# Performance work log

Hardware: AMD Instinct MI355X
Metric: run time of the kernel (lower is better)

The kernel has to match this reference:

```python
import jax, jax.numpy as jnp
import numpy as np

B, T, D = 8, 512, 1024
S, H, TOPK = 2048, 4, 8
Dh = D // H
LR_FAST, LR_DEEP = 1.0, 0.1
SURPRISE_TH, DECAY = 0.6, 0.9995


def layer_norm(x, g, b, eps=1e-5):
    m = jnp.mean(x, -1, keepdims=True)
    v = jnp.var(x, -1, keepdims=True)
    return (x - m) * jax.lax.rsqrt(v + eps) * g + b


def setup_inputs() -> dict:
    key = jax.random.key(0)
    ks = jax.random.split(key, 8)
    s = 0.02
    f32 = jnp.float32
    return {
        "x": jax.random.normal(ks[0], (B, T, D), f32),
        "write_mask": jnp.ones((B, T), dtype=bool),
        # Mamba backbone stub: 2 residual MLP blocks (Linear d->2d, GELU, Linear 2d->d, LN)
        "W1": jax.random.normal(ks[1], (2, D, 2 * D), f32) * s,
        "b1": jnp.zeros((2, 2 * D), f32),
        "W2": jax.random.normal(ks[2], (2, 2 * D, D), f32) * s,
        "b2": jnp.zeros((2, D), f32),
        "ln_g": jnp.ones((2, D), f32),
        "ln_b": jnp.zeros((2, D), f32),
        # memory fusion
        "fuse_W": jax.random.normal(ks[3], (2 * D, D), f32) * s,
        "fuse_b": jnp.zeros((D,), f32),
        "mln_g": jnp.ones((D,), f32),
        "mln_b": jnp.zeros((D,), f32),
        # persistent DualTierMiras memory bank (keys / values)
        "mem_K": jax.random.normal(ks[4], (S, D), f32) * s,
        "mem_V": jax.random.normal(ks[5], (S, D), f32) * s,
    }


def _forward(x, write_mask, W1, b1, W2, b2, ln_g, ln_b, fuse_W, fuse_b, mln_g, mln_b, mem_K, mem_V):
    # --- Mamba backbone (vectorized over B,T) ---
    h = x
    for i in range(2):
        y = jax.nn.gelu(h @ W1[i] + b1[i]) @ W2[i] + b2[i]
        h = h + layer_norm(y, ln_g[i], ln_b[i])

    inv_sqrt_dh = 1.0 / np.sqrt(Dh).astype(np.float32)
    inv_sqrt_d = 1.0 / np.sqrt(D).astype(np.float32)

    def step(carry, inputs):
        mK, mV = carry                      # [S,D] each
        h_t, m_t = inputs                   # [B,D], [B] bool
        # --- top-k sparse multi-head memory read ---
        q = h_t.reshape(B, H, Dh)
        Kh = mK.reshape(S, H, Dh).transpose(1, 0, 2)   # [H,S,Dh]
        Vh = mV.reshape(S, H, Dh).transpose(1, 0, 2)   # [H,S,Dh]
        scores = jnp.einsum('bhd,hsd->bhs', q, Kh) * inv_sqrt_dh  # [B,H,S]
        topv, topi = jax.lax.top_k(scores, TOPK)                   # [B,H,K]
        w = jax.nn.softmax(topv, axis=-1)
        vals = jax.vmap(lambda v, i: v[i])(Vh, topi.transpose(1, 0, 2))  # [H,B,K,Dh]
        v_t = jnp.einsum('bhk,hbkd->bhd', w, vals).reshape(B, D)
        # --- residual fusion ---
        fused = jnp.concatenate([h_t, v_t], -1) @ fuse_W + fuse_b
        fused = layer_norm(fused + h_t, mln_g, mln_b)
        # --- surprise-gated EMA scatter write (detached, decayed) ---
        key_w = jax.lax.stop_gradient(h_t)
        val_w = jax.lax.stop_gradient(fused)
        sw = key_w @ mK.T * inv_sqrt_d                 # [B,S]
        p = jax.nn.softmax(sw, -1)
        slot = jnp.argmax(sw, -1)                      # [B]
        surprise = 1.0 - jnp.max(p, -1)                # [B]
        lr = jnp.where(surprise > SURPRISE_TH, LR_FAST, LR_DEEP)
        lr = lr * m_t.astype(lr.dtype)                 # per-sample write gate
        decay = jnp.where(jnp.any(m_t), DECAY, 1.0)
        mV2 = mV * decay
        mV2 = mV2.at[slot].add(lr[:, None] * (val_w - mV2[slot]))
        mK2 = mK.at[slot].add(lr[:, None] * (key_w - mK[slot]))
        return (mK2, mV2), fused

    (_, _), out = jax.lax.scan(step, (mem_K, mem_V), (h.transpose(1, 0, 2), write_mask.T))
    return out.transpose(1, 0, 2)   # [B,T,D]


def reference(x, write_mask, W1, b1, W2, b2, ln_g, ln_b, fuse_W, fuse_b, mln_g, mln_b, mem_K, mem_V):
    return _forward(x, write_mask, W1, b1, W2, b2, ln_g, ln_b, fuse_W, fuse_b, mln_g, mln_b, mem_K, mem_V)
```

## Files before the change

kernel.cpp:

```cpp
#include <hip/hip_runtime.h>
#include <cstdint>

#define TT 512
#define DD 1024
#define SS 2048
#define BB 8
#define DECAYF 0.9995f
#define NBLK 256

__device__ __forceinline__ float cldf(const float* p) {
  return __hip_atomic_load(p, __ATOMIC_RELAXED, __HIP_MEMORY_SCOPE_AGENT);
}
__device__ __forceinline__ void cstf(float* p, float v) {
  __hip_atomic_store(p, v, __ATOMIC_RELAXED, __HIP_MEMORY_SCOPE_AGENT);
}
__device__ __forceinline__ int cldi(const int* p) {
  return __hip_atomic_load(p, __ATOMIC_RELAXED, __HIP_MEMORY_SCOPE_AGENT);
}
__device__ __forceinline__ void csti(int* p, int v) {
  __hip_atomic_store(p, v, __ATOMIC_RELAXED, __HIP_MEMORY_SCOPE_AGENT);
}

template<int MODE, bool BT>
__global__ __launch_bounds__(256) void gemm64(
    const float* __restrict__ A, int lda,
    const float* __restrict__ B, int ldb,
    const float* __restrict__ bias,
    float* __restrict__ C, int ldc,
    const float* __restrict__ res, int resld,
    int K)
{
  __shared__ float As[16][68];
  __shared__ float Bs[16][68];
  const int tid = threadIdx.x;
  const int m0 = blockIdx.y * 64, n0 = blockIdx.x * 64;
  const int tx = tid & 15, ty = tid >> 4;
  const int a_r = tid >> 2, a_k = (tid & 3) * 4;
  const int b_k = tid >> 4, b_n = (tid & 15) * 4;
  float acc[4][4];
#pragma unroll
  for (int i = 0; i < 4; ++i)
#pragma unroll
    for (int j = 0; j < 4; ++j) acc[i][j] = 0.f;

  for (int k0 = 0; k0 < K; k0 += 16) {
    float4 av = *(const float4*)(A + (size_t)(m0 + a_r) * lda + k0 + a_k);
    As[a_k + 0][a_r] = av.x; As[a_k + 1][a_r] = av.y;
    As[a_k + 2][a_r] = av.z; As[a_k + 3][a_r] = av.w;
    if (!BT) {
      float4 bv = *(const float4*)(B + (size_t)(k0 + b_k) * ldb + n0 + b_n);
      Bs[b_k][b_n + 0] = bv.x; Bs[b_k][b_n + 1] = bv.y;
      Bs[b_k][b_n + 2] = bv.z; Bs[b_k][b_n + 3] = bv.w;
    } else {
      float4 bv = *(const float4*)(B + (size_t)(n0 + a_r) * ldb + k0 + a_k);
      Bs[a_k + 0][a_r] = bv.x; Bs[a_k + 1][a_r] = bv.y;
      Bs[a_k + 2][a_r] = bv.z; Bs[a_k + 3][a_r] = bv.w;
    }
    __syncthreads();
#pragma unroll
    for (int kk = 0; kk < 16; ++kk) {
      float4 a4 = *(const float4*)&As[kk][ty * 4];
      float4 b4 = *(const float4*)&Bs[kk][tx * 4];
      float aa[4] = {a4.x, a4.y, a4.z, a4.w};
      float bb[4] = {b4.x, b4.y, b4.z, b4.w};
#pragma unroll
      for (int i = 0; i < 4; ++i)
#pragma unroll
        for (int j = 0; j < 4; ++j) acc[i][j] += aa[i] * bb[j];
    }
    __syncthreads();
  }
#pragma unroll
  for (int i = 0; i < 4; ++i) {
    const int row = m0 + ty * 4 + i;
    const int col = n0 + tx * 4;
    float v[4];
#pragma unroll
    for (int j = 0; j < 4; ++j) {
      float x = acc[i][j];
      if (MODE == 0 || MODE == 1 || MODE == 3) x += bias[col + j];
      if (MODE == 1) {
        float t3 = x * x * x;
        x = 0.5f * x * (1.f + tanhf(0.7978845608028654f * (x + 0.044715f * t3)));
      }
      if (MODE == 3) x += res[(size_t)row * resld + col + j];
      v[j] = x;
    }
    float4 o; o.x = v[0]; o.y = v[1]; o.z = v[2]; o.w = v[3];
    *(float4*)(C + (size_t)row * ldc + col) = o;
  }
}

__global__ __launch_bounds__(256) void ln_residual(
    const float* __restrict__ Y, float* __restrict__ Hio,
    const float* __restrict__ g, const float* __restrict__ b)
{
  const int row = blockIdx.x, tid = threadIdx.x;
  const int lane = tid & 63, wid = tid >> 6;
  __shared__ float red[8];
  __shared__ float s_m, s_r;
  float x[4]; float ls = 0.f, lq = 0.f;
#pragma unroll
  for (int r = 0; r < 4; ++r) {
    x[r] = Y[(size_t)row * DD + tid + 256 * r];
    ls += x[r]; lq += x[r] * x[r];
  }
#pragma unroll
  for (int off = 32; off; off >>= 1) { ls += __shfl_down(ls, off); lq += __shfl_down(lq, off); }
  if (lane == 0) { red[wid] = ls; red[4 + wid] = lq; }
  __syncthreads();
  if (tid == 0) {
    float S = red[0] + red[1] + red[2] + red[3];
    float Q = red[4] + red[5] + red[6] + red[7];
    float mean = S * (1.f / 1024.f);
    float var = Q * (1.f / 1024.f) - mean * mean;
    s_m = mean; s_r = rsqrtf(var + 1e-5f);
  }
  __syncthreads();
#pragma unroll
  for (int r = 0; r < 4; ++r) {
    int d = tid + 256 * r;
    Hio[(size_t)row * DD + d] += (x[r] - s_m) * s_r * g[d] + b[d];
  }
}

__device__ __forceinline__ void waitn(const int* a, int n, int tgt) {
  if (threadIdx.x < n) {
    while (cldi(&a[threadIdx.x * 32]) < tgt) __builtin_amdgcn_s_sleep(4);
  }
  __syncthreads();
}
__device__ __forceinline__ void arrive1(int* a, int idx, int val) {
  __syncthreads();
  if (threadIdx.x == 0) csti(&a[idx * 32], val);
}

__device__ __forceinline__ void load_qv(float4 (&qv)[8][4], const float* H,
                                        int trow, int lane) {
#pragma unroll
  for (int b = 0; b < 8; ++b)
#pragma unroll
    for (int k = 0; k < 4; ++k)
      qv[b][k] = *(const float4*)(H + ((size_t)b * TT + trow) * DD + lane * 16 + k * 4);
}

__device__ __forceinline__ void compute_scores(
    const float4 (&qv)[8][4], const float* Kl, int bid,
    float* SgP, float* pmxP, float* s_ph, float* s_fd)
{
  const int tid = threadIdx.x, lane = tid & 63, wid = tid >> 6;
  const float4* K4 = (const float4*)Kl;
#pragma unroll
  for (int si = 0; si < 2; ++si) {
    const int sloc = wid * 2 + si;
    float4 kf[4];
#pragma unroll
    for (int k = 0; k < 4; ++k) kf[k] = K4[sloc * 256 + (k << 6) + lane];
    float acc[8];
#pragma unroll
    for (int b = 0; b < 8; ++b) {
      float a = 0.f;
#pragma unroll
      for (int k = 0; k < 4; ++k) {
        a += qv[b][k].x * kf[k].x; a += qv[b][k].y * kf[k].y;
        a += qv[b][k].z * kf[k].z; a += qv[b][k].w * kf[k].w;
      }
      acc[b] = a;
    }
#pragma unroll
    for (int lvl = 1; lvl <= 8; lvl <<= 1)
#pragma unroll
      for (int b = 0; b < 8; ++b) acc[b] += __shfl_xor(acc[b], lvl);
#pragma unroll
    for (int b = 0; b < 8; ++b)
      if ((lane & 15) == b) s_ph[sloc * 32 + (b << 2) + (lane >> 4)] = acc[b];
#pragma unroll
    for (int b = 0; b < 8; ++b) {
      float s1 = acc[b] + __shfl_xor(acc[b], 16);
      s1 += __shfl_xor(s1, 32);
      if (lane == b) s_fd[sloc * 8 + b] = s1;
    }
  }
  __syncthreads();
  {
    const int row = tid >> 3, col = tid & 7;
    cstf(&SgP[(size_t)row * SS + bid * 8 + col], s_ph[col * 32 + row]);
  }
  if (tid < 8) {
    float m = -3e38f; int ix = 0;
#pragma unroll
    for (int s = 0; s < 8; ++s) { float v = s_fd[s * 8 + tid]; if (v > m) { m = v; ix = bid * 8 + s; } }
    float e = 0.f;
#pragma unroll
    for (int s = 0; s < 8; ++s) e += __expf((s_fd[s * 8 + tid] - m) * 0.03125f);
    float* rec = &pmxP[bid * 32];
    cstf(&rec[tid], m); cstf(&rec[8 + tid], e); csti((int*)&rec[16 + tid], ix);
  }
}

__device__ __forceinline__ void fuse_ln_out(
    int b, int tl,
    const float* __restrict__ HP, const float* part,
    float* __restrict__ H, float* pvalP,
    const float* __restrict__ mg, const float* __restrict__ mb,
    float* xr, float* s_red)
{
  const int tid = threadIdx.x;
  const int lane = tid & 63, wid = tid >> 6;
  const size_t row = (size_t)b * TT + tl;
  float ls = 0.f, lq = 0.f;
#pragma unroll
  for (int r = 0; r < 4; ++r) {
    int d = tid + 256 * r;
    float x = HP[row * DD + d]
            + cldf(&part[(0 * 8 + b) * DD + d]) + cldf(&part[(1 * 8 + b) * DD + d])
            + cldf(&part[(2 * 8 + b) * DD + d]) + cldf(&part[(3 * 8 + b) * DD + d]);
    xr[d] = x; ls += x; lq += x * x;
  }
#pragma unroll
  for (int off = 32; off; off >>= 1) { ls += __shfl_down(ls, off); lq += __shfl_down(lq, off); }
  if (lane == 0) { s_red[wid] = ls; s_red[4 + wid] = lq; }
  __syncthreads();
  if (tid == 0) {
    float S = s_red[0] + s_red[1] + s_red[2] + s_red[3];
    float Q = s_red[4] + s_red[5] + s_red[6] + s_red[7];
    float mean = S * (1.f / 1024.f);
    float var = Q * (1.f / 1024.f) - mean * mean;
    s_red[8] = mean; s_red[9] = rsqrtf(var + 1e-5f);
  }
  __syncthreads();
  const float mean = s_red[8], rstd = s_red[9];
#pragma unroll
  for (int r = 0; r < 4; ++r) {
    int d = tid + 256 * r;
    float val = (xr[d] - mean) * rstd * mg[d] + mb[d];
    H[row * DD + d] = val;
    cstf(&pvalP[b * DD + d], val);
  }
}

__global__ __launch_bounds__(256) void scan_kernel(
    float* __restrict__ H, const float* __restrict__ HP, float* U,
    float* Sg3, float* pmx2, float* vt2, float* coefg2, float* part, float* pval2,
    int* arrA, int* arrT, int* arrC, int* arrD, int* arrE,
    const float* __restrict__ memK, const float* __restrict__ fuseW,
    const float* __restrict__ mg, const float* __restrict__ mb)
{
  __shared__ float Kl[8192];
  __shared__ float scr[4352];
  __shared__ float s_ph[256];
  __shared__ float s_fd[64];
  __shared__ float s_red[64];
  __shared__ int   s_redi[32];
  __shared__ float s_M[8];
  __shared__ int   s_MI[8];
  __shared__ float s_tkv[8];
  __shared__ int   s_tki[8];
  __shared__ int   s_ist[2][8];
  __shared__ float s_lr[2][8];

  const int bid = blockIdx.x, tid = threadIdx.x;
  const int lane = tid & 63, wid = tid >> 6;

  if (tid < 8) { s_ist[1][tid] = -1; s_lr[1][tid] = 0.f; }
  {
    float4* K4 = (float4*)Kl;
    const int s0 = bid * 8;
    for (int i = tid; i < 2048; i += 256) {
      int r = i >> 8, c = i & 255;
      K4[r * 256 + ((c & 3) << 6) + (c >> 2)] =
          *(const float4*)(memK + (size_t)(s0 + r) * DD + 4 * c);
    }
  }
  __syncthreads();

  float cr = 1.f;
  float4 qv[8][4];
  load_qv(qv, H, 0, lane);
  compute_scores(qv, Kl, bid, Sg3 , pmx2 , s_ph, s_fd);
  arrive1(arrA, bid, 1);

  for (int t = 0; t < TT; ++t) {
    const int p = t & 1, pp = p ^ 1;
    waitn(arrA, NBLK, t + 1);
    {
      const float* rec = &pmx2[p * 8192 + tid * 32];
      float pm8[8], pe8[8]; int ix8[8];
#pragma unroll
      for (int b = 0; b < 8; ++b) {
        pm8[b] = cldf(&rec[b]); pe8[b] = cldf(&rec[8 + b]);
        ix8[b] = cldi((const int*)&rec[16 + b]);
      }
#pragma unroll
      for (int b = 0; b < 8; ++b) {
        float M = pm8[b]; int MI = ix8[b];
#pragma unroll
        for (int off = 1; off < 64; off <<= 1) {
          float om = __shfl_xor(M, off); int oi = __shfl_xor(MI, off);
          if (om > M || (om == M && oi < MI)) { M = om; MI = oi; }
        }
        if (lane == 0) { s_red[wid * 8 + b] = M; s_redi[wid * 8 + b] = MI; }
      }
      __syncthreads();
      if (tid < 8) {
        float M = s_red[tid]; int MI = s_redi[tid];
#pragma unroll
        for (int w2 = 1; w2 < 4; ++w2) {
          float om = s_red[w2 * 8 + tid]; int oi = s_redi[w2 * 8 + tid];
          if (om > M || (om == M && oi < MI)) { M = om; MI = oi; }
        }
        s_M[tid] = M; s_MI[tid] = MI;
      }
      __syncthreads();
#pragma unroll
      for (int b = 0; b < 8; ++b) {
        float term = pe8[b] * __expf((pm8[b] - s_M[b]) * 0.03125f);
#pragma unroll
        for (int off = 1; off < 64; off <<= 1) term += __shfl_xor(term, off);
        if (lane == 0) s_red[wid * 8 + b] = term;
      }
      __syncthreads();
      if (tid < 8) {
        float seg = s_red[tid] + s_red[8 + tid] + s_red[16 + tid] + s_red[24 + tid];
        float surprise = 1.f - 1.f / seg;
        s_lr[p][tid] = (surprise > 0.6f) ? 1.0f : 0.1f;
        s_ist[p][tid] = s_MI[tid];
      }
      __syncthreads();
    }
    {
      int sl[8]; float lr8[8];
#pragma unroll
      for (int e = 0; e < 8; ++e) { sl[e] = s_ist[p][e]; lr8[e] = s_lr[p][e]; }
      const int s0 = bid * 8;
      float4* K4 = (float4*)Kl;
#pragma unroll
      for (int si = 0; si < 2; ++si) {
        const int sloc = wid * 2 + si, s = s0 + sloc;
        float L = 0.f; bool any = false;
        float4 av[4];
#pragma unroll
        for (int k = 0; k < 4; ++k) { av[k].x = 0.f; av[k].y = 0.f; av[k].z = 0.f; av[k].w = 0.f; }
#pragma unroll
        for (int e = 0; e < 8; ++e) {
          if (sl[e] == s) {
            any = true; L += lr8[e];
#pragma unroll
            for (int k = 0; k < 4; ++k) {
              av[k].x += lr8[e] * qv[e][k].x; av[k].y += lr8[e] * qv[e][k].y;
              av[k].z += lr8[e] * qv[e][k].z; av[k].w += lr8[e] * qv[e][k].w;
            }
          }
        }
        if (any) {
#pragma unroll
          for (int k = 0; k < 4; ++k) {
            float4 kv = K4[sloc * 256 + (k << 6) + lane];
            kv.x = kv.x * (1.f - L) + av[k].x;
            kv.y = kv.y * (1.f - L) + av[k].y;
            kv.z = kv.z * (1.f - L) + av[k].z;
            kv.w = kv.w * (1.f - L) + av[k].w;
            K4[sloc * 256 + (k << 6) + lane] = kv;
          }
        }
      }
    }
    __syncthreads();
    if (t < TT - 1) {
      load_qv(qv, H, t + 1, lane);
      compute_scores(qv, Kl, bid, Sg3 + (size_t)((t + 1) % 3) * 65536,
                     pmx2 + pp * 8192, s_ph, s_fd);
      arrive1(arrA, bid, t + 2);
    }
    if (bid < 32) {
      waitn(arrE, 8, t - 1);
      const float* SgR = &Sg3[(size_t)(t % 3) * 65536 + (size_t)bid * SS];
      float* sc = scr;
#pragma unroll
      for (int j = 0; j < 8; ++j) sc[tid + 256 * j] = cldf(&SgR[tid + 256 * j]);
      __syncthreads();
      if (wid == 0) {
        float a[32];
#pragma unroll
        for (int i = 0; i < 32; ++i) a[i] = sc[lane + 64 * i];
        unsigned msk = 0u;
        for (int r = 0; r < 8; ++r) {
          float bv = -3e38f; int bj = 0;
#pragma unroll
          for (int i = 0; i < 32; ++i) {
            bool ok = !((msk >> i) & 1u) && (a[i] > bv);
            bv = ok ? a[i] : bv;
            bj = ok ? i : bj;
          }
          int bidx = lane + 64 * bj;
#pragma unroll
          for (int off = 1; off < 64; off <<= 1) {
            float ov = __shfl_xor(bv, off);
            int oi = __shfl_xor(bidx, off);
            if (ov > bv || (ov == bv && oi < bidx)) { bv = ov; bidx = oi; }
          }
          if (lane == (bidx & 63)) msk |= 1u << (bidx >> 6);
          if (lane == 0) { s_tkv[r] = bv; s_tki[r] = bidx; }
        }
      }
      __syncthreads();
      float w8[8];
      {
        float mx = s_tkv[0], nrm = 0.f;
#pragma unroll
        for (int j = 0; j < 8; ++j) { w8[j] = __expf((s_tkv[j] - mx) * 0.0625f); nrm += w8[j]; }
        float scale = cr / nrm;
#pragma unroll
        for (int j = 0; j < 8; ++j) w8[j] *= scale;
      }
      int psl[8]; float plr[8];
#pragma unroll
      for (int e = 0; e < 8; ++e) { psl[e] = s_ist[pp][e]; plr[e] = s_lr[pp][e]; }
      const int b = bid >> 2, h = bid & 3;
      float accv = 0.f;
#pragma unroll
      for (int j = 0; j < 8; ++j) {
        int idx = s_tki[j];
        float uval = cldf(&U[(size_t)idx * DD + h * 256 + tid]);
        float L = 0.f;
#pragma unroll
        for (int e = 0; e < 8; ++e) L += (psl[e] == idx) ? plr[e] : 0.f;
        accv += w8[j] * uval * (1.f - L);
      }
      cstf(&vt2[p * 8192 + b * 1024 + h * 256 + tid], accv);
      if (tid < 8) {
        int myslot = psl[tid]; float mylr = plr[tid];
        float ce = 0.f;
#pragma unroll
        for (int j = 0; j < 8; ++j) ce += (s_tki[j] == myslot) ? w8[j] : 0.f;
        cstf(&coefg2[p * 256 + b * 32 + h * 8 + tid], ce * mylr * (1.f / cr));
      }
      arrive1(arrT, bid, t + 1);
    } else if (bid < 96) {
      waitn(arrT, 32, t + 1);
      waitn(arrD, 8, t);
      const int idx = bid - 32, g = idx >> 2, kc = idx & 3;
      float* vtl = scr; float* pr = scr + 2048; float* cfs = scr + 4096;
      cfs[tid] = cldf(&coefg2[p * 256 + tid]);
      float pv[8];
#pragma unroll
      for (int e = 0; e < 8; ++e) pv[e] = cldf(&pval2[pp * 8192 + e * DD + kc * 256 + tid]);
      __syncthreads();
#pragma unroll
      for (int r = 0; r < 8; ++r) {
        float v = cldf(&vt2[p * 8192 + r * DD + kc * 256 + tid]);
#pragma unroll
        for (int e = 0; e < 8; ++e) v += cfs[r * 32 + kc * 8 + e] * pv[e];
        vtl[r * 256 + tid] = v;
      }
      __syncthreads();
      const int colq = tid & 63, ksub = tid >> 6;
      const int col = 64 * g + colq;
      float acc[8];
#pragma unroll
      for (int b2 = 0; b2 < 8; ++b2) acc[b2] = 0.f;
      const float* W2 = fuseW + (size_t)(DD + kc * 256 + ksub * 64) * DD + col;
      const float* vl = vtl + ksub * 64;
      for (int kk = 0; kk < 64; ++kk) {
        float wv = W2[(size_t)kk * DD];
#pragma unroll
        for (int b2 = 0; b2 < 8; ++b2) acc[b2] += vl[b2 * 256 + kk] * wv;
      }
#pragma unroll
      for (int b2 = 0; b2 < 8; ++b2) pr[ksub * 512 + colq * 8 + b2] = acc[b2];
      __syncthreads();
      if (ksub == 0) {
#pragma unroll
        for (int b2 = 0; b2 < 8; ++b2) {
          float s2 = pr[colq * 8 + b2] + pr[512 + colq * 8 + b2]
                   + pr[1024 + colq * 8 + b2] + pr[1536 + colq * 8 + b2];
          cstf(&part[(kc * 8 + b2) * DD + col], s2);
        }
      }
      arrive1(arrC, idx, t + 1);
    } else if (bid < 104) {
      if (t >= 1) {
        waitn(arrC, 64, t);
        waitn(arrE, 8, t - 2);
        fuse_ln_out(bid - 96, t - 1, HP, part, H, pval2 + pp * 8192, mg, mb, scr, s_red);
        arrive1(arrD, bid - 96, t);
      }
    } else if (bid < 112) {
      if (t >= 1) {
        waitn(arrT, 32, t + 1);
        waitn(arrD, 8, t);
        int sl[8]; float lr8[8];
#pragma unroll
        for (int e2 = 0; e2 < 8; ++e2) { sl[e2] = s_ist[pp][e2]; lr8[e2] = s_lr[pp][e2]; }
        const int e = bid - 104, s = sl[e];
        bool owner = true;
        for (int e2 = 0; e2 < e; ++e2) if (sl[e2] == s) owner = false;
        if (owner) {
          float L = 0.f;
#pragma unroll
          for (int e2 = 0; e2 < 8; ++e2) if (sl[e2] == s) L += lr8[e2];
          const float psv = 1.f / cr;
#pragma unroll
          for (int r = 0; r < 4; ++r) {
            int d = tid + 256 * r;
            float add = 0.f;
#pragma unroll
            for (int e2 = 0; e2 < 8; ++e2)
              if (sl[e2] == s) add += lr8[e2] * cldf(&pval2[pp * 8192 + e2 * DD + d]);
            size_t o = (size_t)s * DD + d;
            cstf(&U[o], cldf(&U[o]) * (1.f - L) + psv * add);
          }
        }
        arrive1(arrE, bid - 104, t);
      }
    }
    cr *= DECAYF;
  }
  if (bid >= 96 && bid < 104) {
    waitn(arrC, 64, TT);
    waitn(arrE, 8, TT - 2);
    fuse_ln_out(bid - 96, TT - 1, HP, part, H, pval2 + ((TT - 1) & 1) * 8192,
                mg, mb, scr, s_red);
  }
}

extern "C" void kernel_launch(void* const* d_in, const int* in_sizes, int n_in,
                              void* d_out, int out_size, void* d_ws, size_t ws_size,
                              hipStream_t stream) {
  (void)in_sizes; (void)n_in; (void)out_size; (void)ws_size;
  const float* x     = (const float*)d_in[0];
  const float* W1    = (const float*)d_in[2];
  const float* b1    = (const float*)d_in[3];
  const float* W2    = (const float*)d_in[4];
  const float* b2    = (const float*)d_in[5];
  const float* lng   = (const float*)d_in[6];
  const float* lnb   = (const float*)d_in[7];
  const float* fuseW = (const float*)d_in[8];
  const float* fuseB = (const float*)d_in[9];
  const float* mlng  = (const float*)d_in[10];
  const float* mlnb  = (const float*)d_in[11];
  const float* memK  = (const float*)d_in[12];
  const float* memV  = (const float*)d_in[13];

  float* H = (float*)d_out;
  char* w = (char*)d_ws;
  float* Y1   = (float*)w;
  float* Y2   = (float*)(w + (size_t)32 * 1024 * 1024);
  float* HP   = (float*)(w + (size_t)48 * 1024 * 1024);
  float* U    = (float*)(w + (size_t)64 * 1024 * 1024);
  float* Sg3  = (float*)(w + (size_t)72 * 1024 * 1024);
  char*  db   = w + (size_t)73 * 1024 * 1024;
  float* pmx2   = (float*)db;
  float* vt2    = (float*)(db + 65536);
  float* coefg2 = (float*)(db + 131072);
  float* part   = (float*)(db + 196608);
  float* pval2  = (float*)(db + 327680);
  char*  fl   = w + (size_t)74 * 1024 * 1024;
  int* arrA = (int*)(fl);
  int* arrT = (int*)(fl + 32768);
  int* arrC = (int*)(fl + 36864);
  int* arrD = (int*)(fl + 45056);
  int* arrE = (int*)(fl + 46080);

  hipMemcpyAsync(H, x, (size_t)BB * TT * DD * sizeof(float),
                 hipMemcpyDeviceToDevice, stream);
  for (int l = 0; l < 2; ++l) {
    gemm64<1, false><<<dim3(32, 64), 256, 0, stream>>>(
        H, 1024, W1 + (size_t)l * 1024 * 2048, 2048, b1 + l * 2048,
        Y1, 2048, nullptr, 0, 1024);
    gemm64<0, false><<<dim3(16, 64), 256, 0, stream>>>(
        Y1, 2048, W2 + (size_t)l * 2048 * 1024, 1024, b2 + l * 1024,
        Y2, 1024, nullptr, 0, 2048);
    ln_residual<<<4096, 256, 0, stream>>>(Y2, H, lng + l * 1024, lnb + l * 1024);
  }
  hipMemsetAsync(fl, 0, 65536, stream);
  hipMemcpyAsync(U, memV, (size_t)8 * 1024 * 1024, hipMemcpyDeviceToDevice, stream);
  gemm64<3, false><<<dim3(16, 64), 256, 0, stream>>>(
      H, 1024, fuseW, 1024, fuseB, HP, 1024, H, 1024, 1024);
  scan_kernel<<<NBLK, 256, 0, stream>>>(H, HP, U,
                                        Sg3, pmx2, vt2, coefg2, part, pval2,
                                        arrA, arrT, arrC, arrD, arrE,
                                        memK, fuseW, mlng, mlnb);
}
```

Before: 15.63 ms.

## Replace per-role flag waits with two grid-wide bitmask barriers per step

Replaces the per-block arrival counters and role-specific waits in the persistent scan kernel with two grid-wide barriers per timestep, each built from per-step bitmask words set with atomicOr. Roles are reassigned so that the top-k reader blocks and the fuse/layernorm blocks run before the mid-step barrier, and the next step's score computation, projection partials and memory-update blocks run after it. The top-k selection now runs as a two-stage per-wave then cross-wave reduction, and buffers drop from triple or double to single copies. The goal is fewer and shorter serial spin-waits on the critical path, at the cost of full-grid synchronisation twice per step and less overlap between stages.

```diff
diff --git a/kernel.cpp b/kernel.cpp
--- a/kernel.cpp
+++ b/kernel.cpp
@@ -16,9 +16,6 @@
 }
 __device__ __forceinline__ int cldi(const int* p) {
   return __hip_atomic_load(p, __ATOMIC_RELAXED, __HIP_MEMORY_SCOPE_AGENT);
-}
-__device__ __forceinline__ void csti(int* p, int v) {
-  __hip_atomic_store(p, v, __ATOMIC_RELAXED, __HIP_MEMORY_SCOPE_AGENT);
 }
 
 template<int MODE, bool BT>
@@ -124,15 +121,17 @@
   }
 }
 
-__device__ __forceinline__ void waitn(const int* a, int n, int tgt) {
-  if (threadIdx.x < n) {
-    while (cldi(&a[threadIdx.x * 32]) < tgt) __builtin_amdgcn_s_sleep(4);
-  }
-  __syncthreads();
-}
-__device__ __forceinline__ void arrive1(int* a, int idx, int val) {
-  __syncthreads();
-  if (threadIdx.x == 0) csti(&a[idx * 32], val);
+__device__ __forceinline__ void barr_arrive(unsigned* bar, int t, int bid) {
+  __syncthreads();
+  if (threadIdx.x == 0)
+    atomicOr(&bar[(size_t)(t * 16 + (bid >> 4)) * 32], 1u << (bid & 15));
+}
+__device__ __forceinline__ void barr_wait(const unsigned* bar, int t) {
+  if (threadIdx.x < 16) {
+    const int* w = (const int*)&bar[(size_t)(t * 16 + threadIdx.x) * 32];
+    while ((cldi(w) & 0xFFFF) != 0xFFFF) __builtin_amdgcn_s_sleep(2);
+  }
+  __syncthreads();
 }
 
 __device__ __forceinline__ void load_qv(float4 (&qv)[8][4], const float* H,
@@ -194,14 +193,15 @@
 #pragma unroll
     for (int s = 0; s < 8; ++s) e += __expf((s_fd[s * 8 + tid] - m) * 0.03125f);
     float* rec = &pmxP[bid * 32];
-    cstf(&rec[tid], m); cstf(&rec[8 + tid], e); csti((int*)&rec[16 + tid], ix);
+    cstf(&rec[tid], m); cstf(&rec[8 + tid], e);
+    __hip_atomic_store((int*)&rec[16 + tid], ix, __ATOMIC_RELAXED, __HIP_MEMORY_SCOPE_AGENT);
   }
 }
 
 __device__ __forceinline__ void fuse_ln_out(
     int b, int tl,
     const float* __restrict__ HP, const float* part,
-    float* __restrict__ H, float* pvalP,
+    float* __restrict__ H, float* pval,
     const float* __restrict__ mg, const float* __restrict__ mb,
     float* xr, float* s_red)
 {
@@ -235,14 +235,14 @@
     int d = tid + 256 * r;
     float val = (xr[d] - mean) * rstd * mg[d] + mb[d];
     H[row * DD + d] = val;
-    cstf(&pvalP[b * DD + d], val);
+    cstf(&pval[b * DD + d], val);
   }
 }
 
 __global__ __launch_bounds__(256) void scan_kernel(
     float* __restrict__ H, const float* __restrict__ HP, float* U,
-    float* Sg3, float* pmx2, float* vt2, float* coefg2, float* part, float* pval2,
-    int* arrA, int* arrT, int* arrC, int* arrD, int* arrE,
+    float* Sg2, float* pmx2, float* vt, float* coefg, float* part, float* pval,
+    unsigned* bar1, unsigned* bar2,
     const float* __restrict__ memK, const float* __restrict__ fuseW,
     const float* __restrict__ mg, const float* __restrict__ mb)
 {
@@ -254,6 +254,8 @@
   __shared__ int   s_redi[32];
   __shared__ float s_M[8];
   __shared__ int   s_MI[8];
+  __shared__ float s_cv[32];
+  __shared__ int   s_ci[32];
   __shared__ float s_tkv[8];
   __shared__ int   s_tki[8];
   __shared__ int   s_ist[2][8];
@@ -277,12 +279,12 @@
   float cr = 1.f;
   float4 qv[8][4];
   load_qv(qv, H, 0, lane);
-  compute_scores(qv, Kl, bid, Sg3 , pmx2 , s_ph, s_fd);
-  arrive1(arrA, bid, 1);
+  compute_scores(qv, Kl, bid, Sg2, pmx2, s_ph, s_fd);
+  barr_arrive(bar1, 0, bid);
 
   for (int t = 0; t < TT; ++t) {
     const int p = t & 1, pp = p ^ 1;
-    waitn(arrA, NBLK, t + 1);
+    barr_wait(bar1, t);
     {
       const float* rec = &pmx2[p * 8192 + tid * 32];
       float pm8[8], pe8[8]; int ix8[8];
@@ -364,43 +366,49 @@
           }
         }
       }
-    }
-    __syncthreads();
-    if (t < TT - 1) {
-      load_qv(qv, H, t + 1, lane);
-      compute_scores(qv, Kl, bid, Sg3 + (size_t)((t + 1) % 3) * 65536,
-                     pmx2 + pp * 8192, s_ph, s_fd);
-      arrive1(arrA, bid, t + 2);
+      __syncthreads();
     }
     if (bid < 32) {
-      waitn(arrE, 8, t - 1);
-      const float* SgR = &Sg3[(size_t)(t % 3) * 65536 + (size_t)bid * SS];
-      float* sc = scr;
-#pragma unroll
-      for (int j = 0; j < 8; ++j) sc[tid + 256 * j] = cldf(&SgR[tid + 256 * j]);
+      const float* SgR = &Sg2[(size_t)p * 65536 + (size_t)bid * SS];
+      float av[8]; int ai[8];
+#pragma unroll
+      for (int i = 0; i < 8; ++i) {
+        ai[i] = wid * 512 + lane + 64 * i;
+        av[i] = cldf(&SgR[ai[i]]);
+      }
+      unsigned msk = 0u;
+      for (int r = 0; r < 8; ++r) {
+        float bv = -3e38f; int bj = 0;
+#pragma unroll
+        for (int i = 0; i < 8; ++i) {
+          bool ok = !((msk >> i) & 1u) && (av[i] > bv);
+          bv = ok ? av[i] : bv; bj = ok ? i : bj;
+        }
+        int bidx = ai[bj];
+        float wv = bv; int wi = bidx;
+#pragma unroll
+        for (int off = 1; off < 64; off <<= 1) {
+          float ov = __shfl_xor(wv, off); int oi = __shfl_xor(wi, off);
+          if (ov > wv || (ov == wv && oi < wi)) { wv = ov; wi = oi; }
+        }
+        if (bidx == wi) msk |= 1u << bj;
+        if (lane == 0) { s_cv[wid * 8 + r] = wv; s_ci[wid * 8 + r] = wi; }
+      }
       __syncthreads();
       if (wid == 0) {
-        float a[32];
-#pragma unroll
-        for (int i = 0; i < 32; ++i) a[i] = sc[lane + 64 * i];
-        unsigned msk = 0u;
+        float cv = (lane < 32) ? s_cv[lane] : -3e38f;
+        int   ci = (lane < 32) ? s_ci[lane] : 0x7FFFFFFF;
+        bool used = false;
         for (int r = 0; r < 8; ++r) {
-          float bv = -3e38f; int bj = 0;
-#pragma unroll
-          for (int i = 0; i < 32; ++i) {
-            bool ok = !((msk >> i) & 1u) && (a[i] > bv);
-            bv = ok ? a[i] : bv;
-            bj = ok ? i : bj;
+          float wv = used ? -3e38f : cv;
+          int   wi = used ? 0x7FFFFFFF : ci;
+#pragma unroll
+          for (int off = 1; off < 64; off <<= 1) {
+            float ov = __shfl_xor(wv, off); int oi = __shfl_xor(wi, off);
+            if (ov > wv || (ov == wv && oi < wi)) { wv = ov; wi = oi; }
           }
-          int bidx = lane + 64 * bj;
-#pragma unroll
-          for (int off = 1; off < 64; off <<= 1) {
-            float ov = __shfl_xor(bv, off);
-            int oi = __shfl_xor(bidx, off);
-            if (ov > bv || (ov == bv && oi < bidx)) { bv = ov; bidx = oi; }
-          }
-          if (lane == (bidx & 63)) msk |= 1u << (bidx >> 6);
-          if (lane == 0) { s_tkv[r] = bv; s_tki[r] = bidx; }
+          if (!used && ci == wi) used = true;
+          if (lane == 0) { s_tkv[r] = wv; s_tki[r] = wi; }
         }
       }
       __syncthreads();
@@ -427,28 +435,35 @@
         for (int e = 0; e < 8; ++e) L += (psl[e] == idx) ? plr[e] : 0.f;
         accv += w8[j] * uval * (1.f - L);
       }
-      cstf(&vt2[p * 8192 + b * 1024 + h * 256 + tid], accv);
+      cstf(&vt[b * DD + h * 256 + tid], accv);
       if (tid < 8) {
         int myslot = psl[tid]; float mylr = plr[tid];
         float ce = 0.f;
 #pragma unroll
         for (int j = 0; j < 8; ++j) ce += (s_tki[j] == myslot) ? w8[j] : 0.f;
-        cstf(&coefg2[p * 256 + b * 32 + h * 8 + tid], ce * mylr * (1.f / cr));
-      }
-      arrive1(arrT, bid, t + 1);
-    } else if (bid < 96) {
-      waitn(arrT, 32, t + 1);
-      waitn(arrD, 8, t);
-      const int idx = bid - 32, g = idx >> 2, kc = idx & 3;
+        cstf(&coefg[b * 32 + h * 8 + tid], ce * mylr * (1.f / cr));
+      }
+    } else if (bid < 40) {
+      if (t >= 1) fuse_ln_out(bid - 32, t - 1, HP, part, H, pval, mg, mb, scr, s_red);
+    }
+    barr_arrive(bar2, t, bid);
+    barr_wait(bar2, t);
+    if (t < TT - 1) {
+      load_qv(qv, H, t + 1, lane);
+      compute_scores(qv, Kl, bid, Sg2 + (size_t)pp * 65536,
+                     pmx2 + pp * 8192, s_ph, s_fd);
+    }
+    if (bid >= 64 && bid < 128) {
+      const int idx = bid - 64, g = idx >> 2, kc = idx & 3;
       float* vtl = scr; float* pr = scr + 2048; float* cfs = scr + 4096;
-      cfs[tid] = cldf(&coefg2[p * 256 + tid]);
+      cfs[tid] = cldf(&coefg[tid]);
       float pv[8];
 #pragma unroll
-      for (int e = 0; e < 8; ++e) pv[e] = cldf(&pval2[pp * 8192 + e * DD + kc * 256 + tid]);
+      for (int e = 0; e < 8; ++e) pv[e] = cldf(&pval[e * DD + kc * 256 + tid]);
       __syncthreads();
 #pragma unroll
       for (int r = 0; r < 8; ++r) {
-        float v = cldf(&vt2[p * 8192 + r * DD + kc * 256 + tid]);
+        float v = cldf(&vt[r * DD + kc * 256 + tid]);
 #pragma unroll
         for (int e = 0; e < 8; ++e) v += cfs[r * 32 + kc * 8 + e] * pv[e];
         vtl[r * 256 + tid] = v;
@@ -477,22 +492,12 @@
           cstf(&part[(kc * 8 + b2) * DD + col], s2);
         }
       }
-      arrive1(arrC, idx, t + 1);
-    } else if (bid < 104) {
+    } else if (bid >= 128 && bid < 136) {
       if (t >= 1) {
-        waitn(arrC, 64, t);
-        waitn(arrE, 8, t - 2);
-        fuse_ln_out(bid - 96, t - 1, HP, part, H, pval2 + pp * 8192, mg, mb, scr, s_red);
-        arrive1(arrD, bid - 96, t);
-      }
-    } else if (bid < 112) {
-      if (t >= 1) {
-        waitn(arrT, 32, t + 1);
-        waitn(arrD, 8, t);
         int sl[8]; float lr8[8];
 #pragma unroll
         for (int e2 = 0; e2 < 8; ++e2) { sl[e2] = s_ist[pp][e2]; lr8[e2] = s_lr[pp][e2]; }
-        const int e = bid - 104, s = sl[e];
+        const int e = bid - 128, s = sl[e];
         bool owner = true;
         for (int e2 = 0; e2 < e; ++e2) if (sl[e2] == s) owner = false;
         if (owner) {
@@ -506,21 +511,19 @@
             float add = 0.f;
 #pragma unroll
             for (int e2 = 0; e2 < 8; ++e2)
-              if (sl[e2] == s) add += lr8[e2] * cldf(&pval2[pp * 8192 + e2 * DD + d]);
+              if (sl[e2] == s) add += lr8[e2] * cldf(&pval[e2 * DD + d]);
             size_t o = (size_t)s * DD + d;
             cstf(&U[o], cldf(&U[o]) * (1.f - L) + psv * add);
           }
         }
-        arrive1(arrE, bid - 104, t);
-      }
-    }
+      }
+    }
+    barr_arrive(bar1, t + 1, bid);
     cr *= DECAYF;
   }
-  if (bid >= 96 && bid < 104) {
-    waitn(arrC, 64, TT);
-    waitn(arrE, 8, TT - 2);
-    fuse_ln_out(bid - 96, TT - 1, HP, part, H, pval2 + ((TT - 1) & 1) * 8192,
-                mg, mb, scr, s_red);
+  if (bid >= 32 && bid < 40) {
+    barr_wait(bar1, TT);
+    fuse_ln_out(bid - 32, TT - 1, HP, part, H, pval, mg, mb, scr, s_red);
   }
 }
 
@@ -544,23 +547,19 @@
 
   float* H = (float*)d_out;
   char* w = (char*)d_ws;
-  float* Y1   = (float*)w;
-  float* Y2   = (float*)(w + (size_t)32 * 1024 * 1024);
-  float* HP   = (float*)(w + (size_t)48 * 1024 * 1024);
-  float* U    = (float*)(w + (size_t)64 * 1024 * 1024);
-  float* Sg3  = (float*)(w + (size_t)72 * 1024 * 1024);
-  char*  db   = w + (size_t)73 * 1024 * 1024;
-  float* pmx2   = (float*)db;
-  float* vt2    = (float*)(db + 65536);
-  float* coefg2 = (float*)(db + 131072);
-  float* part   = (float*)(db + 196608);
-  float* pval2  = (float*)(db + 327680);
-  char*  fl   = w + (size_t)74 * 1024 * 1024;
-  int* arrA = (int*)(fl);
-  int* arrT = (int*)(fl + 32768);
-  int* arrC = (int*)(fl + 36864);
-  int* arrD = (int*)(fl + 45056);
-  int* arrE = (int*)(fl + 46080);
+  float*    Y1    = (float*)w;
+  float*    Y2    = (float*)(w + (size_t)32 * 1024 * 1024);
+  float*    HP    = (float*)(w + (size_t)48 * 1024 * 1024);
+  float*    U     = (float*)(w + (size_t)64 * 1024 * 1024);
+  float*    Sg2   = (float*)(w + (size_t)72 * 1024 * 1024);
+  char*     db    = w + (size_t)73 * 1024 * 1024;
+  float*    pmx2  = (float*)db;
+  float*    vt    = (float*)(db + 65536);
+  float*    coefg = (float*)(db + 98304);
+  float*    part  = (float*)(db + 131072);
+  float*    pval  = (float*)(db + 262144);
+  unsigned* bar1  = (unsigned*)(w + (size_t)75 * 1024 * 1024);
+  unsigned* bar2  = (unsigned*)(w + (size_t)77 * 1024 * 1024);
 
   hipMemcpyAsync(H, x, (size_t)BB * TT * DD * sizeof(float),
                  hipMemcpyDeviceToDevice, stream);
@@ -573,12 +572,12 @@
         Y2, 1024, nullptr, 0, 2048);
     ln_residual<<<4096, 256, 0, stream>>>(Y2, H, lng + l * 1024, lnb + l * 1024);
   }
-  hipMemsetAsync(fl, 0, 65536, stream);
+  hipMemsetAsync(bar1, 0, (size_t)4 * 1024 * 1024, stream);
   hipMemcpyAsync(U, memV, (size_t)8 * 1024 * 1024, hipMemcpyDeviceToDevice, stream);
   gemm64<3, false><<<dim3(16, 64), 256, 0, stream>>>(
       H, 1024, fuseW, 1024, fuseB, HP, 1024, H, 1024, 1024);
   scan_kernel<<<NBLK, 256, 0, stream>>>(H, HP, U,
-                                        Sg3, pmx2, vt2, coefg2, part, pval2,
-                                        arrA, arrT, arrC, arrD, arrE,
+                                        Sg2, pmx2, vt, coefg, part, pval,
+                                        bar1, bar2,
                                         memK, fuseW, mlng, mlnb);
 }
```

After: 24.50 ms. 1.57x slower.
